# Kernel optimization log

Measured on AMD Instinct MI355X. Metric: run time of the kernel, lower is better.

The kernel has to match this reference:

```python
import jax, jax.numpy as jnp
import numpy as np
import math

EPS = 1e-5

def _ln(x, g, b):
    m = jnp.mean(x, axis=-1, keepdims=True)
    v = jnp.var(x, axis=-1, keepdims=True)
    return (x - m) * jax.lax.rsqrt(v + EPS) * g + b

def _rn_layer(x, W, g, b, A, Bb, Rw):
    # x: (B,S,in) -> (B,S,out). W: (out,in), A: (out,basis), Bb: (basis,out)
    S = x.shape[1]
    basis_dim = Bb.shape[0]
    n = _ln(x @ W.T, g, b)                      # (B,S,out)
    j = jnp.arange(S) % basis_dim               # (S,)
    Bv = Bb[j]                                  # (S,out)
    scal = jnp.einsum('bsd,sd->bs', n, Bv)      # (B,S)
    Av = A[:, j].T                              # (S,out)
    nf = scal[..., None] * Av                   # (B,S,out)
    res = x if Rw is None else x @ Rw.T
    return nf + res

def _ts_layer(x, M, g, b, P, Rw):
    # x: (B,S,in) -> (B,S,out). M: (out,in), P: (out,out,G)
    S = x.shape[1]
    D, _, G = P.shape
    t = _ln(x @ M.T, g, b)                      # (B,S,out)
    k = jnp.arange(S, dtype=jnp.float32)
    periods = (jnp.arange(D, dtype=jnp.float32)[:, None, None] * (D * G)
               + jnp.arange(D, dtype=jnp.float32)[None, :, None] * G
               + jnp.arange(G, dtype=jnp.float32)[None, None, :] + 2.0)  # (D,D,G)
    phi = jnp.cos(2.0 * math.pi * k[:, None, None, None] / periods)       # (S,D,D,G)
    # Nk[b,s,i] = sum_{j,g} P[i,j,g] * t[b,s,j] * phi[s,i,j,g]
    Wp = jnp.einsum('ijg,sijg->sij', P, phi)    # (S,D,D)
    Nk = jnp.einsum('sij,bsj->bsi', Wp, t)      # (B,S,D)
    return Nk + x @ Rw.T

def setup_inputs() -> dict:
    key = jax.random.key(0)
    ks = jax.random.split(key, 16)
    B, S = 2, 2048
    d0, d1, d2 = 512, 64, 512        # input_dim, ts out, final out
    bas1, G, bas3 = 64, 8, 64
    u = lambda k, sh, a: jax.random.uniform(k, sh, jnp.float32, -a, a)
    inp = {
        'x':  jax.random.normal(ks[0], (B, S, d0), jnp.float32),
        # Layer 1: RN 512->512 (in==out -> no residual proj)
        'W1': u(ks[1], (d0, d0), 0.1),
        'g1': jnp.ones((d0,), jnp.float32),
        'b1': jnp.zeros((d0,), jnp.float32),
        'A1': u(ks[2], (d0, bas1), 0.1),
        'B1': u(ks[3], (bas1, d0), 0.1),
        # Layer 2: TS 512->64
        'M2': u(ks[4], (d1, d0), 0.5),
        'g2': jnp.ones((d1,), jnp.float32),
        'b2': jnp.zeros((d1,), jnp.float32),
        'P2': u(ks[5], (d1, d1, G), 0.1),
        'R2': u(ks[6], (d1, d0), 0.1),
        # Layer 3: RN 64->512
        'W3': u(ks[7], (d2, d1), 0.1),
        'g3': jnp.ones((d2,), jnp.float32),
        'b3': jnp.zeros((d2,), jnp.float32),
        'A3': u(ks[8], (d2, bas3), 0.1),
        'B3': u(ks[9], (bas3, d2), 0.1),
        'R3': u(ks[10], (d2, d1), 0.1),
    }
    return inp

def reference(x, W1, g1, b1, A1, B1, M2, g2, b2, P2, R2, W3, g3, b3, A3, B3, R3):
    h = _rn_layer(x, W1, g1, b1, A1, B1, None)   # (B,S,512), identity residual
    h = _ts_layer(h, M2, g2, b2, P2, R2)         # (B,S,64)
    h = _rn_layer(h, W3, g3, b3, A3, B3, R3)     # (B,S,512)
    return h
```

## Files before the change

### kernel.cpp

```cpp
#include <hip/hip_runtime.h>
#include <math.h>

#define SEQ  2048
#define ROWS 4096
#define D0   512
#define D1   64
#define C2S  524288

typedef short bf8 __attribute__((ext_vector_type(8)));
typedef float f4  __attribute__((ext_vector_type(4)));

__device__ __forceinline__ unsigned short f2bf(float f) {
    unsigned u = __float_as_uint(f);
    return (unsigned short)((u + 0x7fffu + ((u >> 16) & 1u)) >> 16);
}
__device__ __forceinline__ float bf2f(unsigned short u) {
    return __uint_as_float((unsigned)u << 16);
}
__device__ __forceinline__ void hilo(float f, unsigned short& h, unsigned short& l) {
    h = f2bf(f);
    float fh = bf2f(h);
    l = f2bf(f - fh);
}
__device__ __forceinline__ void cv4h(unsigned short* dh, int idx, float4 v) {
    ushort4 hv;
    hv.x = f2bf(v.x); hv.y = f2bf(v.y); hv.z = f2bf(v.z); hv.w = f2bf(v.w);
    *(ushort4*)(dh + idx) = hv;
}

__device__ __forceinline__ void async16(const void* g, void* l) {
    __builtin_amdgcn_global_load_lds(
        (const __attribute__((address_space(1))) unsigned int*)g,
        (__attribute__((address_space(3))) unsigned int*)l, 16, 0, 0);
}

__global__ __launch_bounds__(256) void convk(
        const float* __restrict__ x,  const float* __restrict__ W1,
        const float* __restrict__ M2, const float* __restrict__ R2,
        const float* __restrict__ W3, const float* __restrict__ R3,
        const float* __restrict__ A1, const float* __restrict__ A3,
        unsigned short* __restrict__ xh, unsigned short* __restrict__ xl,
        unsigned short* __restrict__ W1h,
        unsigned short* __restrict__ C2h,
        unsigned short* __restrict__ C3h,
        float* __restrict__ A3T,
        float* __restrict__ G2y, float* __restrict__ G2r) {
    __shared__ float sh[4][64];
    int c = blockIdx.x, tid = threadIdx.x;
    if (c < 1024) {
        int base = c * 2048 + tid * 4;
        float4 v0 = *(const float4*)(x + base);
        float4 v1 = *(const float4*)(x + base + 1024);
        ushort4 h, l;
        hilo(v0.x, h.x, l.x); hilo(v0.y, h.y, l.y);
        hilo(v0.z, h.z, l.z); hilo(v0.w, h.w, l.w);
        *(ushort4*)(xh + base) = h; *(ushort4*)(xl + base) = l;
        hilo(v1.x, h.x, l.x); hilo(v1.y, h.y, l.y);
        hilo(v1.z, h.z, l.z); hilo(v1.w, h.w, l.w);
        *(ushort4*)(xh + base + 1024) = h; *(ushort4*)(xl + base + 1024) = l;
    } else if (c < 1216) {
        const float* src; unsigned short* dh; int off;
        if      (c < 1152) { src = W1; dh = W1h;         off = c - 1024; }
        else if (c < 1168) { src = M2; dh = C2h;         off = c - 1152; }
        else if (c < 1184) { src = R2; dh = C2h + 32768; off = c - 1168; }
        else if (c < 1200) { src = W3; dh = C3h;         off = c - 1184; }
        else               { src = R3; dh = C3h + 32768; off = c - 1200; }
        int base = off * 2048 + tid * 4;
        cv4h(dh, base,        *(const float4*)(src + base));
        cv4h(dh, base + 1024, *(const float4*)(src + base + 1024));
    } else if (c < 1344) {
        int gid = (c - 1216) * 256 + tid;
        int i = gid >> 6, j = gid & 63;
        A3T[j * 512 + i] = A3[gid];
    } else {
        int jrow = (c - 1344) & 63;
        const float* wv = (c < 1408) ? (M2 + jrow * 512) : (R2 + jrow * 512);
        float* G = (c < 1408) ? G2y : G2r;
        int jm = tid & 63, q = tid >> 6;
        const float* ap = A1 + (q * 128) * 64 + jm;
        const float* wp = wv + q * 128;
        float acc = 0.f;
        for (int cc = 0; cc < 128; ++cc)
            acc = fmaf(ap[cc * 64], wp[cc], acc);
        sh[q][jm] = acc;
        __syncthreads();
        if (tid < 64)
            G[tid * 64 + jrow] = (sh[0][tid] + sh[1][tid]) + (sh[2][tid] + sh[3][tid]);
    }
}

template<int AMODE, int OM>
__global__ __launch_bounds__(256, 4) void gemm128t(
        const unsigned short* __restrict__ Ah, const unsigned short* __restrict__ Al,
        const unsigned short* __restrict__ Wh,
        float* __restrict__ Cf, unsigned short* __restrict__ Cb,
        int N, int K, int Ks) {
    __shared__ __align__(16) unsigned short aH[8192];
    __shared__ __align__(16) unsigned short aL[AMODE ? 8192 : 16];
    __shared__ __align__(16) unsigned short wHs[4096];
    const int tid = threadIdx.x;
    const int wv  = tid >> 6;
    const int ln  = tid & 63;
    const int lm  = ln & 15;
    const int lq  = ln >> 4;
    const int bm  = blockIdx.y * 128;
    const int bn  = blockIdx.x * 64;
    const int k0  = blockIdx.z * Ks;
    const bool alo = (AMODE == 1) || (AMODE == 2 && bn >= 512);

    f4 acc[2][4] = {};

    for (int kt = 0; kt < Ks; kt += 64) {
        const int kg = k0 + kt;
        __syncthreads();
#pragma unroll
        for (int i = 0; i < 4; ++i) {
            int slot = i * 256 + wv * 64 + ln;
            int row  = slot >> 3;
            int ch   = (slot & 7) ^ (row & 7);
            size_t go = (size_t)(bm + row) * K + kg + ch * 8;
            async16(Ah + go, aH + slot * 8);
            if (alo) async16(Al + go, aL + slot * 8);
        }
#pragma unroll
        for (int i = 0; i < 2; ++i) {
            int slot = i * 256 + wv * 64 + ln;
            int row  = slot >> 3;
            int ch   = (slot & 7) ^ (row & 7);
            size_t go = (size_t)(bn + row) * K + kg + ch * 8;
            async16(Wh + go, wHs + slot * 8);
        }
        __syncthreads();

#pragma unroll
        for (int kk = 0; kk < 2; ++kk) {
            const int ck = kk * 4 + lq;
            bf8 a_h[2], a_l[2], b_h[4];
#pragma unroll
            for (int t = 0; t < 2; ++t) {
                int r = wv * 32 + t * 16 + lm;
                a_h[t] = *(const bf8*)(aH + r * 64 + ((ck ^ (r & 7)) * 8));
                if (alo)
                    a_l[t] = *(const bf8*)(aL + r * 64 + ((ck ^ (r & 7)) * 8));
            }
#pragma unroll
            for (int u = 0; u < 4; ++u) {
                int rb = u * 16 + lm;
                b_h[u] = *(const bf8*)(wHs + rb * 64 + ((ck ^ (rb & 7)) * 8));
            }
#pragma unroll
            for (int t = 0; t < 2; ++t)
#pragma unroll
                for (int u = 0; u < 4; ++u) {
                    acc[t][u] = __builtin_amdgcn_mfma_f32_16x16x32_bf16(a_h[t], b_h[u], acc[t][u], 0, 0, 0);
                    if (alo)
                        acc[t][u] = __builtin_amdgcn_mfma_f32_16x16x32_bf16(a_l[t], b_h[u], acc[t][u], 0, 0, 0);
                }
        }
    }

#pragma unroll
    for (int t = 0; t < 2; ++t)
#pragma unroll
        for (int u = 0; u < 4; ++u) {
            int row = bm + wv * 32 + t * 16 + lq * 4;
            int col = bn + u * 16 + lm;
#pragma unroll
            for (int r = 0; r < 4; ++r) {
                float v = acc[t][u][r];
                if (col < 512)
                    Cb[(size_t)blockIdx.z * ROWS * 512 + (size_t)(row + r) * 512 + col] = f2bf(v);
                else
                    Cf[(size_t)blockIdx.z * ROWS * 128 + (size_t)(row + r) * 128 + (col - 512)] = v;
            }
        }
}

__global__ __launch_bounds__(256) void ptk(
        const unsigned short* __restrict__ C1b,
        const float* __restrict__ C2,
        const float* __restrict__ B1,
        const float* __restrict__ g1, const float* __restrict__ b1,
        const float* __restrict__ g2, const float* __restrict__ b2,
        const float* __restrict__ G2y, const float* __restrict__ G2r,
        float* __restrict__ t, float* __restrict__ rsum) {
    const int row = blockIdx.x * 4 + (threadIdx.x >> 6);
    const int l = threadIdx.x & 63;
    const int c = l * 8;
    const int jm = row & 63;
    const size_t rb0 = (size_t)row * 512 + c;
    ushort4 ua = *(const ushort4*)(C1b + rb0);
    ushort4 ub = *(const ushort4*)(C1b + rb0 + 4);
    ushort4 va = *(const ushort4*)(C1b + (size_t)ROWS * 512 + rb0);
    ushort4 vb = *(const ushort4*)(C1b + (size_t)ROWS * 512 + rb0 + 4);
    float y[8];
    y[0] = bf2f(ua.x) + bf2f(va.x); y[1] = bf2f(ua.y) + bf2f(va.y);
    y[2] = bf2f(ua.z) + bf2f(va.z); y[3] = bf2f(ua.w) + bf2f(va.w);
    y[4] = bf2f(ub.x) + bf2f(vb.x); y[5] = bf2f(ub.y) + bf2f(vb.y);
    y[6] = bf2f(ub.z) + bf2f(vb.z); y[7] = bf2f(ub.w) + bf2f(vb.w);
    float4 B0  = *(const float4*)(B1 + jm * 512 + c);
    float4 B1q = *(const float4*)(B1 + jm * 512 + c + 4);
    float4 gg0 = *(const float4*)(g1 + c), gg1 = *(const float4*)(g1 + c + 4);
    float4 bb0 = *(const float4*)(b1 + c), bb1 = *(const float4*)(b1 + c + 4);
    float Bv[8] = {B0.x, B0.y, B0.z, B0.w, B1q.x, B1q.y, B1q.z, B1q.w};
    float gv[8] = {gg0.x, gg0.y, gg0.z, gg0.w, gg1.x, gg1.y, gg1.z, gg1.w};
    float bv[8] = {bb0.x, bb0.y, bb0.z, bb0.w, bb1.x, bb1.y, bb1.z, bb1.w};
    float sum = 0.f, ssq = 0.f, S1 = 0.f, SU = 0.f, SBB = 0.f;
#pragma unroll
    for (int i = 0; i < 8; ++i) {
        float u = gv[i] * Bv[i];
        sum += y[i];
        ssq = fmaf(y[i], y[i], ssq);
        S1  = fmaf(y[i], u, S1);
        SU  += u;
        SBB = fmaf(bv[i], Bv[i], SBB);
    }
#pragma unroll
    for (int m = 1; m < 64; m <<= 1) {
        sum += __shfl_xor(sum, m, 64);
        ssq += __shfl_xor(ssq, m, 64);
        S1  += __shfl_xor(S1, m, 64);
        SU  += __shfl_xor(SU, m, 64);
        SBB += __shfl_xor(SBB, m, 64);
    }
    float mean = sum * (1.0f / 512.0f);
    float var  = ssq * (1.0f / 512.0f) - mean * mean;
    float rstd = rsqrtf(var + 1e-5f);
    float p = rstd * (S1 - mean * SU) + SBB;

    const size_t rb = (size_t)row * 128;
    float z  = C2[rb + l]      + C2[C2S + rb + l];
    float zr = C2[rb + 64 + l] + C2[C2S + rb + 64 + l];
    float v  = z  + p * G2y[jm * 64 + l];
    float rv = zr + p * G2r[jm * 64 + l];
    float s2 = v, q2 = v * v;
#pragma unroll
    for (int m = 1; m < 64; m <<= 1) {
        s2 += __shfl_xor(s2, m, 64);
        q2 += __shfl_xor(q2, m, 64);
    }
    float mean2 = s2 * (1.0f / 64.0f);
    float var2  = q2 * (1.0f / 64.0f) - mean2 * mean2;
    float rstd2 = rsqrtf(var2 + 1e-5f);
    t[row * 64 + l]    = (v - mean2) * rstd2 * g2[l] + b2[l];
    rsum[row * 64 + l] = rv;
}

__global__ __launch_bounds__(256) void tsk2(
        const float* __restrict__ t, const float* __restrict__ rsum,
        const float* __restrict__ P,
        unsigned short* __restrict__ Hh, unsigned short* __restrict__ Hl) {
    const int bid = blockIdx.x;
    const int i   = bid >> 3;
    const int sg  = bid & 7;
    const int w   = threadIdx.x >> 6;
    const int ln  = threadIdx.x & 63;
    const int s0  = sg * 256 + w * 64;
    const int idx = i * 64 + ln;
    const float* pp = P + idx * 8;
    const float sf0 = (float)s0;

    float k2c[8], ca[8], cb[8];
#pragma unroll
    for (int g = 0; g < 8; ++g) {
        float pf   = (float)(idx * 8 + g + 2);
        float invp = __builtin_amdgcn_rcpf(pf);
        k2c[g] = 2.0f * __builtin_amdgcn_cosf(invp);
        float q0 = floorf(sf0 * invp);
        float r0 = fmaf(-q0, pf, sf0);
        float f0 = r0 * invp; f0 -= floorf(f0);
        float c0 = __builtin_amdgcn_cosf(f0);
        float sf1 = sf0 + 1.0f;
        float q1 = floorf(sf1 * invp);
        float r1 = fmaf(-q1, pf, sf1);
        float f1 = r1 * invp; f1 -= floorf(f1);
        float c1 = __builtin_amdgcn_cosf(f1);
        float Pv = pp[g];
        ca[g] = Pv * c0;
        cb[g] = Pv * c1;
    }

    const int tb = s0 * 64 + ln;
    float t0c = t[tb], t1c = t[131072 + tb];
    float res0 = 0.f, res1 = 0.f;

    for (int st = 0; st < 64; st += 2) {
        float t0n  = t[tb + (st + 1) * 64];
        float t1n  = t[131072 + tb + (st + 1) * 64];
        float ws = ((ca[0] + ca[1]) + (ca[2] + ca[3]))
                 + ((ca[4] + ca[5]) + (ca[6] + ca[7]));
#pragma unroll
        for (int g = 0; g < 8; ++g) ca[g] = fmaf(k2c[g], cb[g], -ca[g]);
        float v0 = ws * t0c, v1 = ws * t1c;
#pragma unroll
        for (int m = 1; m < 64; m <<= 1) {
            v0 += __shfl_xor(v0, m, 64);
            v1 += __shfl_xor(v1, m, 64);
        }
        res0 = (ln == st) ? v0 : res0;
        res1 = (ln == st) ? v1 : res1;
        float t0n2 = t[tb + (st + 2) * 64];
        float t1n2 = t[131072 + tb + (st + 2) * 64];
        float ws2 = ((cb[0] + cb[1]) + (cb[2] + cb[3]))
                  + ((cb[4] + cb[5]) + (cb[6] + cb[7]));
#pragma unroll
        for (int g = 0; g < 8; ++g) cb[g] = fmaf(k2c[g], ca[g], -cb[g]);
        float v0b = ws2 * t0n, v1b = ws2 * t1n;
#pragma unroll
        for (int m = 1; m < 64; m <<= 1) {
            v0b += __shfl_xor(v0b, m, 64);
            v1b += __shfl_xor(v1b, m, 64);
        }
        res0 = (ln == st + 1) ? v0b : res0;
        res1 = (ln == st + 1) ? v1b : res1;
        t0c = t0n2; t1c = t1n2;
    }

    const int s = s0 + ln;
    {
        float v = res0 + rsum[(size_t)s * 64 + i];
        unsigned short h, l; hilo(v, h, l);
        Hh[(size_t)s * 64 + i] = h; Hl[(size_t)s * 64 + i] = l;
        float v1e = res1 + rsum[(size_t)(SEQ + s) * 64 + i];
        hilo(v1e, h, l);
        Hh[(size_t)(SEQ + s) * 64 + i] = h; Hl[(size_t)(SEQ + s) * 64 + i] = l;
    }
}

__global__ __launch_bounds__(256) void g3ln(
        const unsigned short* __restrict__ Hh, const unsigned short* __restrict__ Hl,
        const unsigned short* __restrict__ Wc3h,
        const float* __restrict__ g3, const float* __restrict__ b3,
        const float* __restrict__ B3, const float* __restrict__ A3T,
        float* __restrict__ outf) {
    __shared__ __align__(16) unsigned short aH[1024];
    __shared__ __align__(16) unsigned short aL[1024];
    __shared__ __align__(16) unsigned short wS[16384];
    __shared__ float cS[16 * 1024];
    const int tid = threadIdx.x;
    const int wv  = tid >> 6;
    const int ln  = tid & 63;
    const int lm  = ln & 15;
    const int lq  = ln >> 4;
    const int r0  = blockIdx.x * 16;

    {
        int slot = (wv & 1) * 64 + ln;
        int row  = slot >> 3;
        int ch   = (slot & 7) ^ (row & 7);
        size_t go = (size_t)(r0 + row) * 64 + ch * 8;
        if (wv < 2) async16(Hh + go, aH + slot * 8);
        else        async16(Hl + go, aL + slot * 8);
    }

    bf8 ah[2], al[2];
    for (int q = 0; q < 4; ++q) {
#pragma unroll
        for (int i = 0; i < 8; ++i) {
            int slot = i * 256 + tid;
            int lr   = slot >> 3;
            int ch   = (slot & 7) ^ (lr & 7);
            int grow = (lr >> 6) * 256 + q * 64 + (lr & 63);
            size_t go = (size_t)grow * 64 + ch * 8;
            async16(Wc3h + go, wS + slot * 8);
        }
        __syncthreads();
        if (q == 0) {
#pragma unroll
            for (int kk = 0; kk < 2; ++kk) {
                int ck = kk * 4 + lq;
                ah[kk] = *(const bf8*)(aH + lm * 64 + ((ck ^ (lm & 7)) * 8));
                al[kk] = *(const bf8*)(aL + lm * 64 + ((ck ^ (lm & 7)) * 8));
            }
        }
        f4 acc[4] = {};
#pragma unroll
        for (int kk = 0; kk < 2; ++kk) {
            int ck = kk * 4 + lq;
            bf8 bh[4];
#pragma unroll
            for (int u = 0; u < 4; ++u) {
                int lr = wv * 64 + u * 16 + lm;
                bh[u] = *(const bf8*)(wS + lr * 64 + ((ck ^ (lr & 7)) * 8));
            }
#pragma unroll
            for (int u = 0; u < 4; ++u) {
                acc[u] = __builtin_amdgcn_mfma_f32_16x16x32_bf16(ah[kk], bh[u], acc[u], 0, 0, 0);
                acc[u] = __builtin_amdgcn_mfma_f32_16x16x32_bf16(al[kk], bh[u], acc[u], 0, 0, 0);
            }
        }
#pragma unroll
        for (int u = 0; u < 4; ++u) {
            int col = wv * 256 + q * 64 + u * 16 + lm;
#pragma unroll
            for (int r = 0; r < 4; ++r)
                cS[(lq * 4 + r) * 1024 + col] = acc[u][r];
        }
        __syncthreads();
    }

    for (int rr = 0; rr < 4; ++rr) {
        int row  = wv * 4 + rr;
        int grow = r0 + row;
        int jm   = grow & 63;
        const float* Bp = B3  + jm * 512;
        const float* Ap = A3T + jm * 512;
        float sum = 0.f, ssq = 0.f, S1 = 0.f, SU = 0.f, SBB = 0.f;
#pragma unroll
        for (int k = 0; k < 8; ++k) {
            int col = ln + k * 64;
            float y  = cS[row * 1024 + col];
            float Bv = Bp[col];
            float gv = g3[col];
            float bv = b3[col];
            float u = gv * Bv;
            sum += y;
            ssq = fmaf(y, y, ssq);
            S1  = fmaf(y, u, S1);
            SU  += u;
            SBB = fmaf(bv, Bv, SBB);
        }
#pragma unroll
        for (int m = 1; m < 64; m <<= 1) {
            sum += __shfl_xor(sum, m, 64);
            ssq += __shfl_xor(ssq, m, 64);
            S1  += __shfl_xor(S1, m, 64);
            SU  += __shfl_xor(SU, m, 64);
            SBB += __shfl_xor(SBB, m, 64);
        }
        float mean = sum * (1.0f / 512.0f);
        float var  = ssq * (1.0f / 512.0f) - mean * mean;
        float rstd = rsqrtf(var + 1e-5f);
        float p = rstd * (S1 - mean * SU) + SBB;
#pragma unroll
        for (int k = 0; k < 8; ++k) {
            int col = ln + k * 64;
            float res = cS[row * 1024 + 512 + col];
            outf[(size_t)grow * 512 + col] = fmaf(p, Ap[col], res);
        }
    }
}

extern "C" void kernel_launch(void* const* d_in, const int* in_sizes, int n_in,
                              void* d_out, int out_size, void* d_ws, size_t ws_size,
                              hipStream_t stream) {
    (void)in_sizes; (void)n_in; (void)out_size; (void)ws_size;
    const float* x  = (const float*)d_in[0];
    const float* W1 = (const float*)d_in[1];
    const float* g1 = (const float*)d_in[2];
    const float* b1 = (const float*)d_in[3];
    const float* A1 = (const float*)d_in[4];
    const float* B1 = (const float*)d_in[5];
    const float* M2 = (const float*)d_in[6];
    const float* g2 = (const float*)d_in[7];
    const float* b2 = (const float*)d_in[8];
    const float* P2 = (const float*)d_in[9];
    const float* R2 = (const float*)d_in[10];
    const float* W3 = (const float*)d_in[11];
    const float* g3 = (const float*)d_in[12];
    const float* b3 = (const float*)d_in[13];
    const float* A3 = (const float*)d_in[14];
    const float* B3 = (const float*)d_in[15];
    const float* R3 = (const float*)d_in[16];

    float* ws = (float*)d_ws;
    float* C2   = ws;
    float* t    = ws + 4194304;
    float* rsum = ws + 4456448;
    float* G2y  = ws + 4718592;
    float* G2r  = ws + 4722688;
    float* A3T  = ws + 4751360;
    unsigned short* us = (unsigned short*)(ws + 4784128);
    unsigned short* xh   = us;
    unsigned short* xl   = us + 2097152;
    unsigned short* W1h  = us + 6291456;
    unsigned short* Wc2h = us + 6553600;
    unsigned short* Wc3h = us + 6619136;
    unsigned short* h2h  = us + 6684672;
    unsigned short* h2l  = us + 6946816;
    unsigned short* C1b  = us + 7208960;

    dim3 blk(256);

    convk<<<1472, blk, 0, stream>>>(x, W1, M2, R2, W3, R3, A1, A3,
                                    xh, xl, W1h, Wc2h, Wc3h, A3T, G2y, G2r);

    gemm128t<2, 3><<<dim3(10, 32, 2), blk, 0, stream>>>(
        xh, xl, W1h, C2, C1b, 640, 512, 256);

    ptk<<<1024, blk, 0, stream>>>(C1b, C2, B1, g1, b1, g2, b2, G2y, G2r, t, rsum);

    tsk2<<<512, blk, 0, stream>>>(t, rsum, P2, h2h, h2l);

    g3ln<<<256, blk, 0, stream>>>(h2h, h2l, Wc3h, g3, b3, B3, A3T, (float*)d_out);
}
```

Measured before the change: 143.7 us.

## Keep final GEMM accumulators in registers and precompute per-row LN dot constants

Rewrites the final layer-3 kernel so each wave computes 256 output columns (16 MFMA tiles) directly from global memory into registers, dropping the LDS staging of weights and the 64KB LDS result buffer. Waves 0-1 compute LayerNorm statistics and the B3-weighted sum over the normalized half, reduce them via shuffles and a small shared array, and waves 2-3 write the residual half plus the rank-one term. The g3·B3 and b3·B3 row sums are moved into two extra blocks of the setup kernel. This removes large LDS traffic and improves occupancy, at the cost of uncoalesced direct global bf8 loads and high register pressure from 16 accumulators per thread.

```diff
diff --git a/kernel.cpp b/kernel.cpp
--- a/kernel.cpp
+++ b/kernel.cpp
@@ -39,12 +39,15 @@
         const float* __restrict__ M2, const float* __restrict__ R2,
         const float* __restrict__ W3, const float* __restrict__ R3,
         const float* __restrict__ A1, const float* __restrict__ A3,
+        const float* __restrict__ g3, const float* __restrict__ b3,
+        const float* __restrict__ B3,
         unsigned short* __restrict__ xh, unsigned short* __restrict__ xl,
         unsigned short* __restrict__ W1h,
         unsigned short* __restrict__ C2h,
         unsigned short* __restrict__ C3h,
         float* __restrict__ A3T,
-        float* __restrict__ G2y, float* __restrict__ G2r) {
+        float* __restrict__ G2y, float* __restrict__ G2r,
+        float* __restrict__ SU3, float* __restrict__ SBB3) {
     __shared__ float sh[4][64];
     int c = blockIdx.x, tid = threadIdx.x;
     if (c < 1024) {
@@ -72,7 +75,7 @@
         int gid = (c - 1216) * 256 + tid;
         int i = gid >> 6, j = gid & 63;
         A3T[j * 512 + i] = A3[gid];
-    } else {
+    } else if (c < 1472) {
         int jrow = (c - 1344) & 63;
         const float* wv = (c < 1408) ? (M2 + jrow * 512) : (R2 + jrow * 512);
         float* G = (c < 1408) ? G2y : G2r;
@@ -86,6 +89,19 @@
         __syncthreads();
         if (tid < 64)
             G[tid * 64 + jrow] = (sh[0][tid] + sh[1][tid]) + (sh[2][tid] + sh[3][tid]);
+    } else {
+        const float* vec = (c == 1472) ? g3 : b3;
+        float* dst = (c == 1472) ? SU3 : SBB3;
+        int jm = tid >> 2, q = tid & 3;
+        const float* bp = B3 + jm * 512 + q * 128;
+        const float* vp = vec + q * 128;
+        float acc = 0.f;
+        for (int cc = 0; cc < 128; ++cc)
+            acc = fmaf(bp[cc], vp[cc], acc);
+        sh[q][jm] = acc;
+        __syncthreads();
+        if (tid < 64)
+            dst[tid] = (sh[0][tid] + sh[1][tid]) + (sh[2][tid] + sh[3][tid]);
     }
 }
 
@@ -327,16 +343,15 @@
     }
 }
 
-__global__ __launch_bounds__(256) void g3ln(
+__global__ __launch_bounds__(256) void g3r(
         const unsigned short* __restrict__ Hh, const unsigned short* __restrict__ Hl,
         const unsigned short* __restrict__ Wc3h,
-        const float* __restrict__ g3, const float* __restrict__ b3,
+        const float* __restrict__ g3,
         const float* __restrict__ B3, const float* __restrict__ A3T,
+        const float* __restrict__ SU3, const float* __restrict__ SBB3,
         float* __restrict__ outf) {
-    __shared__ __align__(16) unsigned short aH[1024];
-    __shared__ __align__(16) unsigned short aL[1024];
-    __shared__ __align__(16) unsigned short wS[16384];
-    __shared__ float cS[16 * 1024];
+    __shared__ float part[2][16][3];
+    __shared__ float pSh[16];
     const int tid = threadIdx.x;
     const int wv  = tid >> 6;
     const int ln  = tid & 63;
@@ -344,99 +359,89 @@
     const int lq  = ln >> 4;
     const int r0  = blockIdx.x * 16;
 
-    {
-        int slot = (wv & 1) * 64 + ln;
-        int row  = slot >> 3;
-        int ch   = (slot & 7) ^ (row & 7);
-        size_t go = (size_t)(r0 + row) * 64 + ch * 8;
-        if (wv < 2) async16(Hh + go, aH + slot * 8);
-        else        async16(Hl + go, aL + slot * 8);
-    }
-
     bf8 ah[2], al[2];
-    for (int q = 0; q < 4; ++q) {
-#pragma unroll
-        for (int i = 0; i < 8; ++i) {
-            int slot = i * 256 + tid;
-            int lr   = slot >> 3;
-            int ch   = (slot & 7) ^ (lr & 7);
-            int grow = (lr >> 6) * 256 + q * 64 + (lr & 63);
-            size_t go = (size_t)grow * 64 + ch * 8;
-            async16(Wc3h + go, wS + slot * 8);
-        }
-        __syncthreads();
-        if (q == 0) {
-#pragma unroll
-            for (int kk = 0; kk < 2; ++kk) {
-                int ck = kk * 4 + lq;
-                ah[kk] = *(const bf8*)(aH + lm * 64 + ((ck ^ (lm & 7)) * 8));
-                al[kk] = *(const bf8*)(aL + lm * 64 + ((ck ^ (lm & 7)) * 8));
-            }
-        }
-        f4 acc[4] = {};
-#pragma unroll
-        for (int kk = 0; kk < 2; ++kk) {
-            int ck = kk * 4 + lq;
-            bf8 bh[4];
-#pragma unroll
-            for (int u = 0; u < 4; ++u) {
-                int lr = wv * 64 + u * 16 + lm;
-                bh[u] = *(const bf8*)(wS + lr * 64 + ((ck ^ (lr & 7)) * 8));
-            }
-#pragma unroll
-            for (int u = 0; u < 4; ++u) {
-                acc[u] = __builtin_amdgcn_mfma_f32_16x16x32_bf16(ah[kk], bh[u], acc[u], 0, 0, 0);
-                acc[u] = __builtin_amdgcn_mfma_f32_16x16x32_bf16(al[kk], bh[u], acc[u], 0, 0, 0);
-            }
-        }
-#pragma unroll
-        for (int u = 0; u < 4; ++u) {
-            int col = wv * 256 + q * 64 + u * 16 + lm;
-#pragma unroll
-            for (int r = 0; r < 4; ++r)
-                cS[(lq * 4 + r) * 1024 + col] = acc[u][r];
-        }
-        __syncthreads();
-    }
-
-    for (int rr = 0; rr < 4; ++rr) {
-        int row  = wv * 4 + rr;
-        int grow = r0 + row;
-        int jm   = grow & 63;
-        const float* Bp = B3  + jm * 512;
-        const float* Ap = A3T + jm * 512;
-        float sum = 0.f, ssq = 0.f, S1 = 0.f, SU = 0.f, SBB = 0.f;
-#pragma unroll
-        for (int k = 0; k < 8; ++k) {
-            int col = ln + k * 64;
-            float y  = cS[row * 1024 + col];
-            float Bv = Bp[col];
+#pragma unroll
+    for (int kk = 0; kk < 2; ++kk) {
+        int ck = kk * 4 + lq;
+        ah[kk] = *(const bf8*)(Hh + (size_t)(r0 + lm) * 64 + ck * 8);
+        al[kk] = *(const bf8*)(Hl + (size_t)(r0 + lm) * 64 + ck * 8);
+    }
+
+    f4 acc[16];
+#pragma unroll
+    for (int u = 0; u < 16; ++u) acc[u] = (f4){0.f, 0.f, 0.f, 0.f};
+#pragma unroll
+    for (int kk = 0; kk < 2; ++kk) {
+        int ck = kk * 4 + lq;
+#pragma unroll
+        for (int u = 0; u < 16; ++u) {
+            int wrow = wv * 256 + u * 16 + lm;
+            bf8 bh = *(const bf8*)(Wc3h + (size_t)wrow * 64 + ck * 8);
+            acc[u] = __builtin_amdgcn_mfma_f32_16x16x32_bf16(ah[kk], bh, acc[u], 0, 0, 0);
+            acc[u] = __builtin_amdgcn_mfma_f32_16x16x32_bf16(al[kk], bh, acc[u], 0, 0, 0);
+        }
+    }
+
+    if (wv < 2) {
+        float pr_sum[4] = {0.f, 0.f, 0.f, 0.f};
+        float pr_ssq[4] = {0.f, 0.f, 0.f, 0.f};
+        float pr_s1[4]  = {0.f, 0.f, 0.f, 0.f};
+#pragma unroll
+        for (int u = 0; u < 16; ++u) {
+            int col = wv * 256 + u * 16 + lm;
             float gv = g3[col];
-            float bv = b3[col];
-            float u = gv * Bv;
-            sum += y;
-            ssq = fmaf(y, y, ssq);
-            S1  = fmaf(y, u, S1);
-            SU  += u;
-            SBB = fmaf(bv, Bv, SBB);
-        }
-#pragma unroll
-        for (int m = 1; m < 64; m <<= 1) {
-            sum += __shfl_xor(sum, m, 64);
-            ssq += __shfl_xor(ssq, m, 64);
-            S1  += __shfl_xor(S1, m, 64);
-            SU  += __shfl_xor(SU, m, 64);
-            SBB += __shfl_xor(SBB, m, 64);
-        }
+#pragma unroll
+            for (int r = 0; r < 4; ++r) {
+                float y = acc[u][r];
+                int jm = (r0 + lq * 4 + r) & 63;
+                float Bv = B3[jm * 512 + col];
+                pr_sum[r] += y;
+                pr_ssq[r] = fmaf(y, y, pr_ssq[r]);
+                pr_s1[r]  = fmaf(y, gv * Bv, pr_s1[r]);
+            }
+        }
+#pragma unroll
+        for (int m = 1; m < 16; m <<= 1) {
+#pragma unroll
+            for (int r = 0; r < 4; ++r) {
+                pr_sum[r] += __shfl_xor(pr_sum[r], m, 64);
+                pr_ssq[r] += __shfl_xor(pr_ssq[r], m, 64);
+                pr_s1[r]  += __shfl_xor(pr_s1[r], m, 64);
+            }
+        }
+        if (lm == 0) {
+#pragma unroll
+            for (int r = 0; r < 4; ++r) {
+                part[wv][lq * 4 + r][0] = pr_sum[r];
+                part[wv][lq * 4 + r][1] = pr_ssq[r];
+                part[wv][lq * 4 + r][2] = pr_s1[r];
+            }
+        }
+    }
+    __syncthreads();
+    if (tid < 16) {
+        float sum = part[0][tid][0] + part[1][tid][0];
+        float ssq = part[0][tid][1] + part[1][tid][1];
+        float S1  = part[0][tid][2] + part[1][tid][2];
+        int jm = (r0 + tid) & 63;
         float mean = sum * (1.0f / 512.0f);
         float var  = ssq * (1.0f / 512.0f) - mean * mean;
         float rstd = rsqrtf(var + 1e-5f);
-        float p = rstd * (S1 - mean * SU) + SBB;
-#pragma unroll
-        for (int k = 0; k < 8; ++k) {
-            int col = ln + k * 64;
-            float res = cS[row * 1024 + 512 + col];
-            outf[(size_t)grow * 512 + col] = fmaf(p, Ap[col], res);
+        pSh[tid] = rstd * (S1 - mean * SU3[jm]) + SBB3[jm];
+    }
+    __syncthreads();
+
+    if (wv >= 2) {
+#pragma unroll
+        for (int u = 0; u < 16; ++u) {
+            int ocol = (wv - 2) * 256 + u * 16 + lm;
+#pragma unroll
+            for (int r = 0; r < 4; ++r) {
+                int row = lq * 4 + r;
+                int jm = (r0 + row) & 63;
+                outf[(size_t)(r0 + row) * 512 + ocol] =
+                    fmaf(pSh[row], A3T[jm * 512 + ocol], acc[u][r]);
+            }
         }
     }
 }
@@ -469,6 +474,8 @@
     float* rsum = ws + 4456448;
     float* G2y  = ws + 4718592;
     float* G2r  = ws + 4722688;
+    float* SU3  = ws + 4726784;
+    float* SBB3 = ws + 4726912;
     float* A3T  = ws + 4751360;
     unsigned short* us = (unsigned short*)(ws + 4784128);
     unsigned short* xh   = us;
@@ -482,8 +489,9 @@
 
     dim3 blk(256);
 
-    convk<<<1472, blk, 0, stream>>>(x, W1, M2, R2, W3, R3, A1, A3,
-                                    xh, xl, W1h, Wc2h, Wc3h, A3T, G2y, G2r);
+    convk<<<1474, blk, 0, stream>>>(x, W1, M2, R2, W3, R3, A1, A3, g3, b3, B3,
+                                    xh, xl, W1h, Wc2h, Wc3h, A3T,
+                                    G2y, G2r, SU3, SBB3);
 
     gemm128t<2, 3><<<dim3(10, 32, 2), blk, 0, stream>>>(
         xh, xl, W1h, C2, C1b, 640, 512, 256);
@@ -492,5 +500,6 @@
 
     tsk2<<<512, blk, 0, stream>>>(t, rsum, P2, h2h, h2l);
 
-    g3ln<<<256, blk, 0, stream>>>(h2h, h2l, Wc3h, g3, b3, B3, A3T, (float*)d_out);
-}
+    g3r<<<256, blk, 0, stream>>>(h2h, h2l, Wc3h, g3, B3, A3T, SU3, SBB3,
+                                 (float*)d_out);
+}
```

After: 151.1 us. 5.2% more time.
